# Optimization experiments

Measured on AMD Instinct MI355X. Metric: run time of the kernel, lower is better.

## Reference

```python
import jax, jax.numpy as jnp
import numpy as np

B, N = 128, 512
D_MODEL = 512
N_EXPERTS = 8
N_ELEM = 4   # VALID_ELEMENTS = range(4)
N_CHG = 3    # VALID_CHARGES = range(-1, 2); stored as index 0..2


def setup_inputs() -> dict:
    key = jax.random.key(0)
    ks = jax.random.split(key, 9)
    s = 1.0 / np.sqrt(D_MODEL)  # torch nn.Linear default init bound
    X = jax.random.normal(ks[0], (B, N, D_MODEL), jnp.float32)
    E = jax.random.randint(ks[1], (B, N), 0, N_ELEM)          # element label per atom
    C = jax.random.randint(ks[2], (B, N), 0, N_CHG)           # charge-label index per atom
    Wg = jax.random.uniform(ks[3], (D_MODEL, N_EXPERTS), jnp.float32, -s, s)
    bg = jax.random.uniform(ks[4], (N_EXPERTS,), jnp.float32, -s, s)
    # per-expert, per-label scalar projections (the only weights reaching the output)
    We = jax.random.uniform(ks[5], (N_EXPERTS, N_ELEM, D_MODEL), jnp.float32, -s, s)
    be = jax.random.uniform(ks[6], (N_EXPERTS, N_ELEM), jnp.float32, -s, s)
    Wc = jax.random.uniform(ks[7], (N_EXPERTS, N_CHG, D_MODEL), jnp.float32, -s, s)
    bc = jax.random.uniform(ks[8], (N_EXPERTS, N_CHG), jnp.float32, -s, s)
    return {"X": X, "E": E, "C": C, "Wg": Wg, "bg": bg,
            "We": We, "be": be, "Wc": Wc, "bc": bc}


def reference(X, E, C, Wg, bg, We, be, Wc, bc):
    # Gating: softmax over experts per atom, summed over atoms -> [B, X]
    gate = jax.nn.softmax(X @ Wg + bg, axis=-1).sum(axis=1)

    # Label-routed scalar projections, computed for all labels then selected
    # (matches the source's compute-all-then-torch.where semantics; at selected
    # positions X_masked == X, so applying the linear to full X is identical).
    pe_all = jnp.einsum('bnd,xld->bnxl', X, We) + be          # [B,N,X,4]
    pc_all = jnp.einsum('bnd,xld->bnxl', X, Wc) + bc          # [B,N,X,3]
    pe = (pe_all * jax.nn.one_hot(E, N_ELEM, dtype=X.dtype)[:, :, None, :]).sum(-1)  # [B,N,X]
    pc = (pc_all * jax.nn.one_hot(C, N_CHG, dtype=X.dtype)[:, :, None, :]).sum(-1)   # [B,N,X]

    # per_atom_IE = pe * |pc|; expert returns -(per_atom_IE).sum over atoms
    expert_out = -(pe * jnp.abs(pc)).sum(axis=1)              # [B, X]
    return (gate * expert_out).sum(axis=-1)                   # [B]
```

## Files before the change

kernel.cpp:

```cpp
#include <hip/hip_runtime.h>


#define WPACK_OFF 0
#define BIAS_OFF  65536
#define G_OFF     66560
#define S_OFF     70656

typedef __bf16 bf16x8 __attribute__((ext_vector_type(8)));
typedef float  f32x4  __attribute__((ext_vector_type(4)));

__global__ __launch_bounds__(256) void prep_kernel(
    const float* __restrict__ Wg, const float* __restrict__ bg,
    const float* __restrict__ We, const float* __restrict__ be,
    const float* __restrict__ Wc, const float* __restrict__ bc,
    unsigned char* __restrict__ ws)
{
    int tid = blockIdx.x * 256 + threadIdx.x;
    __bf16* wpack = (__bf16*)(ws + WPACK_OFF);
    float*  bias  = (float*)(ws + BIAS_OFF);

    if (tid < 32768) {
        int j    = tid & 7;
        int lane = (tid >> 3) & 63;
        int ni   = (tid >> 9) & 3;
        int kc   = tid >> 11;
        int col  = ni * 16 + (lane & 15);
        int k    = kc * 32 + (lane >> 4) * 8 + j;
        float v;
        if (col < 8)       v = Wg[k * 8 + col];
        else if (col < 40) v = We[(col - 8) * 512 + k];
        else               v = Wc[(col - 40) * 512 + k];
        wpack[tid] = (__bf16)v;
    } else if (tid < 32832) {
        int col = tid - 32768;
        float v;
        if (col < 8)       v = bg[col];
        else if (col < 40) v = be[col - 8];
        else               v = bc[col - 40];
        bias[col] = v;
    }
}

__device__ inline bf16x8 load_conv(const float* __restrict__ p) {
    float4 u = *(const float4*)p;
    float4 v = *(const float4*)(p + 4);
    bf16x8 r;
    r[0] = (__bf16)u.x; r[1] = (__bf16)u.y; r[2] = (__bf16)u.z; r[3] = (__bf16)u.w;
    r[4] = (__bf16)v.x; r[5] = (__bf16)v.y; r[6] = (__bf16)v.z; r[7] = (__bf16)v.w;
    return r;
}

__global__ __launch_bounds__(256) void moe_main(
    const float* __restrict__ X, const int* __restrict__ E, const int* __restrict__ C,
    unsigned char* __restrict__ ws,
    float* __restrict__ G, float* __restrict__ S)
{
    __shared__ float ylds[4][16 * 65];
    __shared__ float bias_s[64];
    __shared__ float gacc[8], sacc[8];

    const int tid  = threadIdx.x;
    const int wave = tid >> 6;
    const int lane = tid & 63;
    const int quad = lane >> 4;
    const int l16  = lane & 15;

    if (tid < 64) bias_s[tid] = *((const float*)(ws + BIAS_OFF) + tid);
    if (tid < 8) { gacc[tid] = 0.0f; sacc[tid] = 0.0f; }

    const int atom0 = blockIdx.x * 32;
    const int b     = blockIdx.x >> 4;
    const int tile  = wave >> 1;
    const int khalf = wave & 1;
    const int kbase = khalf * 8;
    const int atomT = atom0 + tile * 16;

    const bf16x8* __restrict__ wp = (const bf16x8*)(ws + WPACK_OFF);

    const float* xr = X + (size_t)(atomT + l16) * 512 + quad * 8;

    f32x4 acc[4];
    #pragma unroll
    for (int ni = 0; ni < 4; ++ni) acc[ni] = 0.0f;

    bf16x8 a0 = load_conv(xr + kbase * 32);
    bf16x8 a1 = load_conv(xr + (kbase + 1) * 32);
    #pragma unroll
    for (int i = 0; i < 8; ++i) {
        const int kc = kbase + i;
        const bf16x8* wpk = wp + kc * 256 + lane;
        bf16x8 b0 = wpk[0];
        bf16x8 b1 = wpk[64];
        bf16x8 b2 = wpk[128];
        bf16x8 b3 = wpk[192];
        bf16x8 a2 = a1;
        if (i < 6) a2 = load_conv(xr + (kc + 2) * 32);
        acc[0] = __builtin_amdgcn_mfma_f32_16x16x32_bf16(a0, b0, acc[0], 0, 0, 0);
        acc[1] = __builtin_amdgcn_mfma_f32_16x16x32_bf16(a0, b1, acc[1], 0, 0, 0);
        acc[2] = __builtin_amdgcn_mfma_f32_16x16x32_bf16(a0, b2, acc[2], 0, 0, 0);
        acc[3] = __builtin_amdgcn_mfma_f32_16x16x32_bf16(a0, b3, acc[3], 0, 0, 0);
        a0 = a1;
        a1 = a2;
    }

    float* Y = ylds[wave];
    #pragma unroll
    for (int ni = 0; ni < 4; ++ni)
        #pragma unroll
        for (int r = 0; r < 4; ++r)
            Y[(quad * 4 + r) * 65 + ni * 16 + l16] = acc[ni][r];
    __syncthreads();

    if ((wave & 1) == 0) {
        float Gv[8], Sv[8];
        #pragma unroll
        for (int x = 0; x < 8; ++x) { Gv[x] = 0.0f; Sv[x] = 0.0f; }

        if (lane < 16) {
            const int atom = atomT + lane;
            const int e = E[atom];
            const int c = C[atom];
            const float* y0 = ylds[wave]     + lane * 65;
            const float* y1 = ylds[wave + 1] + lane * 65;

            float lg[8], m = -1e30f;
            #pragma unroll
            for (int x = 0; x < 8; ++x) {
                lg[x] = y0[x] + y1[x] + bias_s[x];
                m = fmaxf(m, lg[x]);
            }
            float sum = 0.0f;
            #pragma unroll
            for (int x = 0; x < 8; ++x) {
                lg[x] = __expf(lg[x] - m);
                sum += lg[x];
            }
            float inv = 1.0f / sum;
            #pragma unroll
            for (int x = 0; x < 8; ++x) {
                Gv[x] = lg[x] * inv;
                int ie = 8 + x * 4 + e, ic = 40 + x * 3 + c;
                float pe = y0[ie] + y1[ie] + bias_s[ie];
                float pc = y0[ic] + y1[ic] + bias_s[ic];
                Sv[x] = pe * fabsf(pc);
            }
        }

        #pragma unroll
        for (int x = 0; x < 8; ++x) {
            float g = Gv[x], s = Sv[x];
            #pragma unroll
            for (int off = 8; off > 0; off >>= 1) {
                g += __shfl_down(g, off);
                s += __shfl_down(s, off);
            }
            if (lane == 0) {
                atomicAdd(&gacc[x], g);
                atomicAdd(&sacc[x], s);
            }
        }
    }
    __syncthreads();
    if (tid < 8) {
        atomicAdd(&G[b * 8 + tid], gacc[tid]);
        atomicAdd(&S[b * 8 + tid], sacc[tid]);
    }
}

__global__ void final_kernel(const unsigned char* __restrict__ ws,
                             float* __restrict__ out)
{
    int b = threadIdx.x;
    const float* G = (const float*)(ws + G_OFF);
    const float* S = (const float*)(ws + S_OFF);
    if (b < 128) {
        float s = 0.0f;
        #pragma unroll
        for (int x = 0; x < 8; ++x) s += G[b * 8 + x] * S[b * 8 + x];
        out[b] = -s;
    }
}

extern "C" void kernel_launch(void* const* d_in, const int* in_sizes, int n_in,
                              void* d_out, int out_size, void* d_ws, size_t ws_size,
                              hipStream_t stream) {
    const float* X  = (const float*)d_in[0];
    const int*   E  = (const int*)d_in[1];
    const int*   C  = (const int*)d_in[2];
    const float* Wg = (const float*)d_in[3];
    const float* bg = (const float*)d_in[4];
    const float* We = (const float*)d_in[5];
    const float* be = (const float*)d_in[6];
    const float* Wc = (const float*)d_in[7];
    const float* bc = (const float*)d_in[8];
    unsigned char* ws = (unsigned char*)d_ws;
    float* out = (float*)d_out;

    float* G = (float*)(ws + G_OFF);
    float* S = (float*)(ws + S_OFF);

    hipLaunchKernelGGL(prep_kernel, dim3(129), dim3(256), 0, stream,
                       Wg, bg, We, be, Wc, bc, ws);
    hipLaunchKernelGGL(moe_main, dim3(2048), dim3(256), 0, stream,
                       X, E, C, ws, G, S);
    hipLaunchKernelGGL(final_kernel, dim3(1), dim3(128), 0, stream, ws, out);
}
```

Before: 209.6 us.

## Give each wave full-K ownership of 16 atoms and parallelize epilogue across lanes

Each wave now computes the full 512-long K reduction for its own 16 atoms instead of splitting K across wave pairs, so a block handles 64 atoms and the grid halves. The A-operand prefetch depth grows from two chunks to four. The epilogue spreads work over all 64 lanes (4 lanes per atom, 2 experts each) with shuffle-based softmax and reductions, replacing a 16-lane serial path. This removes the cross-wave partial-sum merge and the idle waves in the epilogue, at the cost of higher register use and a longer serial MFMA chain per wave.

```diff
diff --git a/kernel.cpp b/kernel.cpp
--- a/kernel.cpp
+++ b/kernel.cpp
@@ -68,39 +68,36 @@
     if (tid < 64) bias_s[tid] = *((const float*)(ws + BIAS_OFF) + tid);
     if (tid < 8) { gacc[tid] = 0.0f; sacc[tid] = 0.0f; }
 
-    const int atom0 = blockIdx.x * 32;
-    const int b     = blockIdx.x >> 4;
-    const int tile  = wave >> 1;
-    const int khalf = wave & 1;
-    const int kbase = khalf * 8;
-    const int atomT = atom0 + tile * 16;
+    const int atomW = blockIdx.x * 64 + wave * 16;
+    const int b     = blockIdx.x >> 3;
 
     const bf16x8* __restrict__ wp = (const bf16x8*)(ws + WPACK_OFF);
 
-    const float* xr = X + (size_t)(atomT + l16) * 512 + quad * 8;
+    const float* xr = X + (size_t)(atomW + l16) * 512 + quad * 8;
 
     f32x4 acc[4];
     #pragma unroll
     for (int ni = 0; ni < 4; ++ni) acc[ni] = 0.0f;
 
-    bf16x8 a0 = load_conv(xr + kbase * 32);
-    bf16x8 a1 = load_conv(xr + (kbase + 1) * 32);
+    bf16x8 a0 = load_conv(xr);
+    bf16x8 a1 = load_conv(xr + 32);
+    bf16x8 a2 = load_conv(xr + 64);
+    bf16x8 a3 = load_conv(xr + 96);
+
     #pragma unroll
-    for (int i = 0; i < 8; ++i) {
-        const int kc = kbase + i;
+    for (int kc = 0; kc < 16; ++kc) {
         const bf16x8* wpk = wp + kc * 256 + lane;
         bf16x8 b0 = wpk[0];
         bf16x8 b1 = wpk[64];
         bf16x8 b2 = wpk[128];
         bf16x8 b3 = wpk[192];
-        bf16x8 a2 = a1;
-        if (i < 6) a2 = load_conv(xr + (kc + 2) * 32);
+        bf16x8 an = a3;
+        if (kc < 12) an = load_conv(xr + (kc + 4) * 32);
         acc[0] = __builtin_amdgcn_mfma_f32_16x16x32_bf16(a0, b0, acc[0], 0, 0, 0);
         acc[1] = __builtin_amdgcn_mfma_f32_16x16x32_bf16(a0, b1, acc[1], 0, 0, 0);
         acc[2] = __builtin_amdgcn_mfma_f32_16x16x32_bf16(a0, b2, acc[2], 0, 0, 0);
         acc[3] = __builtin_amdgcn_mfma_f32_16x16x32_bf16(a0, b3, acc[3], 0, 0, 0);
-        a0 = a1;
-        a1 = a2;
+        a0 = a1; a1 = a2; a2 = a3; a3 = an;
     }
 
     float* Y = ylds[wave];
@@ -111,54 +108,44 @@
             Y[(quad * 4 + r) * 65 + ni * 16 + l16] = acc[ni][r];
     __syncthreads();
 
-    if ((wave & 1) == 0) {
-        float Gv[8], Sv[8];
-        #pragma unroll
-        for (int x = 0; x < 8; ++x) { Gv[x] = 0.0f; Sv[x] = 0.0f; }
+    const int a  = lane >> 2;
+    const int g  = lane & 3;
+    const int x0 = 2 * g, x1 = 2 * g + 1;
+    const float* Yr = Y + a * 65;
+    const int atom = atomW + a;
+    const int e = E[atom];
+    const int c = C[atom];
 
-        if (lane < 16) {
-            const int atom = atomT + lane;
-            const int e = E[atom];
-            const int c = C[atom];
-            const float* y0 = ylds[wave]     + lane * 65;
-            const float* y1 = ylds[wave + 1] + lane * 65;
+    float lg0 = Yr[x0] + bias_s[x0];
+    float lg1 = Yr[x1] + bias_s[x1];
+    float m = fmaxf(lg0, lg1);
+    m = fmaxf(m, __shfl_xor(m, 1));
+    m = fmaxf(m, __shfl_xor(m, 2));
+    float e0 = __expf(lg0 - m);
+    float e1 = __expf(lg1 - m);
+    float sden = e0 + e1;
+    sden += __shfl_xor(sden, 1);
+    sden += __shfl_xor(sden, 2);
+    float inv = 1.0f / sden;
+    float G0 = e0 * inv, G1 = e1 * inv;
 
-            float lg[8], m = -1e30f;
-            #pragma unroll
-            for (int x = 0; x < 8; ++x) {
-                lg[x] = y0[x] + y1[x] + bias_s[x];
-                m = fmaxf(m, lg[x]);
-            }
-            float sum = 0.0f;
-            #pragma unroll
-            for (int x = 0; x < 8; ++x) {
-                lg[x] = __expf(lg[x] - m);
-                sum += lg[x];
-            }
-            float inv = 1.0f / sum;
-            #pragma unroll
-            for (int x = 0; x < 8; ++x) {
-                Gv[x] = lg[x] * inv;
-                int ie = 8 + x * 4 + e, ic = 40 + x * 3 + c;
-                float pe = y0[ie] + y1[ie] + bias_s[ie];
-                float pc = y0[ic] + y1[ic] + bias_s[ic];
-                Sv[x] = pe * fabsf(pc);
-            }
-        }
+    const int ie0 = 8 + x0 * 4 + e, ic0 = 40 + x0 * 3 + c;
+    const int ie1 = 8 + x1 * 4 + e, ic1 = 40 + x1 * 3 + c;
+    float S0 = (Yr[ie0] + bias_s[ie0]) * fabsf(Yr[ic0] + bias_s[ic0]);
+    float S1 = (Yr[ie1] + bias_s[ie1]) * fabsf(Yr[ic1] + bias_s[ic1]);
 
-        #pragma unroll
-        for (int x = 0; x < 8; ++x) {
-            float g = Gv[x], s = Sv[x];
-            #pragma unroll
-            for (int off = 8; off > 0; off >>= 1) {
-                g += __shfl_down(g, off);
-                s += __shfl_down(s, off);
-            }
-            if (lane == 0) {
-                atomicAdd(&gacc[x], g);
-                atomicAdd(&sacc[x], s);
-            }
-        }
+    #pragma unroll
+    for (int off = 32; off >= 4; off >>= 1) {
+        G0 += __shfl_down(G0, off);
+        G1 += __shfl_down(G1, off);
+        S0 += __shfl_down(S0, off);
+        S1 += __shfl_down(S1, off);
+    }
+    if (lane < 4) {
+        atomicAdd(&gacc[2 * lane],     G0);
+        atomicAdd(&gacc[2 * lane + 1], G1);
+        atomicAdd(&sacc[2 * lane],     S0);
+        atomicAdd(&sacc[2 * lane + 1], S1);
     }
     __syncthreads();
     if (tid < 8) {
@@ -201,7 +188,7 @@
 
     hipLaunchKernelGGL(prep_kernel, dim3(129), dim3(256), 0, stream,
                        Wg, bg, We, be, Wc, bc, ws);
-    hipLaunchKernelGGL(moe_main, dim3(2048), dim3(256), 0, stream,
+    hipLaunchKernelGGL(moe_main, dim3(1024), dim3(256), 0, stream,
                        X, E, C, ws, G, S);
     hipLaunchKernelGGL(final_kernel, dim3(1), dim3(128), 0, stream, ws, out);
 }
```

After: 210.8 us. No clear change (+0.6%).
